# Kernel optimization log

Measured on AMD Instinct MI355X. Metric: run time of the kernel, lower is better.

The kernel has to match this reference:

```python
import jax, jax.numpy as jnp
import numpy as np

KERNEL_MUL = 2.0
KERNEL_NUM = 5


def _mmd(source, target):
    n = source.shape[0]
    total = jnp.concatenate([source, target], axis=0)          # [2N, D]
    n_samples = total.shape[0]
    # GEMM-based pairwise squared L2 distances (same math as broadcast subtract/square/sum)
    sq = jnp.sum(total * total, axis=-1)                        # [2N]
    L2 = sq[:, None] + sq[None, :] - 2.0 * (total @ total.T)    # [2N, 2N]
    # bandwidth from detached distances (torch uses .data)
    bw = jax.lax.stop_gradient(jnp.sum(L2)) / (n_samples ** 2 - n_samples)
    bw = bw / (KERNEL_MUL ** (KERNEL_NUM // 2))
    kernels = jnp.zeros_like(L2)
    for i in range(KERNEL_NUM):
        kernels = kernels + jnp.exp(-L2 / (bw * KERNEL_MUL ** i))
    XX = kernels[:n, :n]
    YY = kernels[n:, n:]
    XY = kernels[:n, n:]
    YX = kernels[n:, :n]
    return jnp.mean(XX + YY - XY - YX)


def setup_inputs() -> dict:
    key = jax.random.key(0)
    k1, k2 = jax.random.split(key)
    N, D = 4096, 128
    source = jax.random.normal(k1, (N, D), dtype=jnp.float32)
    target = jax.random.normal(k2, (N, D), dtype=jnp.float32)
    return {"source": source, "target": target}


def reference(source, target):
    return _mmd(source, target)
```

## Files before the change

### kernel.cpp

```cpp
#include <hip/hip_runtime.h>

#define D 128
#define N_TILES 2080

typedef __attribute__((ext_vector_type(8))) short short8;
typedef __attribute__((ext_vector_type(4))) float float4v;

static __device__ __forceinline__ unsigned short f2bf(float f) {
    unsigned int u = __float_as_uint(f);
    unsigned int r = (u + 0x7fffu + ((u >> 16) & 1u)) >> 16;
    return (unsigned short)r;
}

template <bool STORE>
__global__ void k_rowsq_convert(const float* __restrict__ src, const float* __restrict__ tgt,
                                float* __restrict__ rowsq, unsigned int* __restrict__ xbf) {
    int wave = threadIdx.x >> 6, lane = threadIdx.x & 63;
    int r = blockIdx.x * 4 + wave;
    const float* Xr = (r < 4096) ? src + (size_t)r * D : tgt + (size_t)(r - 4096) * D;
    float2 f = ((const float2*)Xr)[lane];
    float s = f.x * f.x + f.y * f.y;
    if (STORE) {
        unsigned int lo = f2bf(f.x), hi = f2bf(f.y);
        xbf[r * 64 + lane] = lo | (hi << 16);
    }
    #pragma unroll
    for (int off = 32; off; off >>= 1) s += __shfl_down(s, off);
    if (lane == 0) rowsq[r] = s;
}

__global__ void p2_colpart(const float* __restrict__ src, const float* __restrict__ tgt,
                           float* __restrict__ colpart) {
    int b = blockIdx.x;
    int col = threadIdx.x & 127, half = threadIdx.x >> 7;
    const float* X = (b < 64) ? src + (size_t)(b * 64) * D : tgt + (size_t)((b - 64) * 64) * D;
    float part = 0.f;
    for (int i = 0; i < 32; ++i) part += X[(size_t)(2 * i + half) * D + col];
    __shared__ float cp[2][128];
    cp[half][col] = part;
    __syncthreads();
    if (threadIdx.x < 128) colpart[b * 128 + threadIdx.x] = cp[0][threadIdx.x] + cp[1][threadIdx.x];
}

__global__ void p3_consts(const float* __restrict__ rowsq, const float* __restrict__ colpart,
                          float* __restrict__ wsf) {
    int tid = threadIdx.x;
    __shared__ float red[8];
    float s = 0.f;
    for (int i = 0; i < 32; ++i) s += rowsq[tid + 256 * i];
    #pragma unroll
    for (int off = 32; off; off >>= 1) s += __shfl_down(s, off);
    if ((tid & 63) == 0) red[tid >> 6] = s;
    __syncthreads();
    float sumsq = red[0] + red[1] + red[2] + red[3];

    float v = 0.f;
    if (tid < 128) {
        float sd = 0.f;
        for (int b = 0; b < 128; ++b) sd += colpart[b * 128 + tid];
        v = sd * sd;
    }
    __syncthreads();
    #pragma unroll
    for (int off = 32; off; off >>= 1) v += __shfl_down(v, off);
    if ((tid & 63) == 0) red[4 + (tid >> 6)] = v;
    __syncthreads();
    if (tid == 0) {
        double s2 = (double)red[4] + red[5] + red[6] + red[7];
        double sumL2 = 2.0 * 8192.0 * (double)sumsq - 2.0 * s2;
        double bw = sumL2 / (8192.0 * 8192.0 - 8192.0) / 4.0;
        wsf[4] = (float)(-1.4426950408889634 / (bw * 16.0));
    }
}

template <bool BF16WS>
__global__ __launch_bounds__(256, 2) void mmd_main(const float* __restrict__ src,
                                                   const float* __restrict__ tgt,
                                                   const unsigned short* __restrict__ xbf,
                                                   const float* __restrict__ rowsq,
                                                   const float* __restrict__ wsf,
                                                   float* __restrict__ partial) {
    __shared__ unsigned short ldsA[128 * D];
    __shared__ unsigned short ldsB[128 * D];

    int t = blockIdx.x;
    int bi = (int)((129.0 - sqrt(129.0 * 129.0 - 8.0 * (double)t)) * 0.5);
    auto base = [](int b) { return (b * (129 - b)) >> 1; };
    while (base(bi + 1) <= t) ++bi;
    while (base(bi) > t) --bi;
    int bj = bi + (t - base(bi));

    const int tid = threadIdx.x, lane = tid & 63, wv = tid >> 6;
    const int quad = lane >> 4, mrow = lane & 15;

    if (BF16WS) {
        const unsigned short* XA = xbf + (size_t)bi * 128 * D;
        const unsigned short* XB = xbf + (size_t)bj * 128 * D;
        #pragma unroll
        for (int j = 0; j < 8; ++j) {
            int slot = wv * 512 + j * 64 + lane;
            int rr = slot >> 4, sc = slot & 15;
            int cc = sc ^ (rr & 7);
            const unsigned short* gA = XA + rr * D + cc * 8;
            const unsigned short* gB = XB + rr * D + cc * 8;
            int lbase = (wv * 512 + j * 64) * 8;
            __builtin_amdgcn_global_load_lds((const __attribute__((address_space(1))) void*)gA,
                                             (__attribute__((address_space(3))) void*)&ldsA[lbase],
                                             16, 0, 0);
            __builtin_amdgcn_global_load_lds((const __attribute__((address_space(1))) void*)gB,
                                             (__attribute__((address_space(3))) void*)&ldsB[lbase],
                                             16, 0, 0);
        }
    } else {
        const float* XA = (bi < 32) ? src + (size_t)bi * 128 * D : tgt + (size_t)(bi - 32) * 128 * D;
        const float* XB = (bj < 32) ? src + (size_t)bj * 128 * D : tgt + (size_t)(bj - 32) * 128 * D;
        #pragma unroll
        for (int j = 0; j < 8; ++j) {
            int id = j * 256 + tid;
            int rr = id >> 4, cc = id & 15;
            const float4* pa = (const float4*)(XA + rr * D + cc * 8);
            const float4* pb = (const float4*)(XB + rr * D + cc * 8);
            float4 a0 = pa[0], a1 = pa[1];
            float4 b0 = pb[0], b1 = pb[1];
            int dst = rr * D + (cc ^ (rr & 7)) * 8;
            union { unsigned short u[8]; uint4 v; } ka, kb;
            ka.u[0] = f2bf(a0.x); ka.u[1] = f2bf(a0.y); ka.u[2] = f2bf(a0.z); ka.u[3] = f2bf(a0.w);
            ka.u[4] = f2bf(a1.x); ka.u[5] = f2bf(a1.y); ka.u[6] = f2bf(a1.z); ka.u[7] = f2bf(a1.w);
            kb.u[0] = f2bf(b0.x); kb.u[1] = f2bf(b0.y); kb.u[2] = f2bf(b0.z); kb.u[3] = f2bf(b0.w);
            kb.u[4] = f2bf(b1.x); kb.u[5] = f2bf(b1.y); kb.u[6] = f2bf(b1.z); kb.u[7] = f2bf(b1.w);
            *(uint4*)&ldsA[dst] = ka.v;
            *(uint4*)&ldsB[dst] = kb.v;
        }
    }
    float c4 = wsf[4];
    __syncthreads();

    const int wm = wv & 1, wn = wv >> 1;

    float4v accf[4][4];
    #pragma unroll
    for (int mt = 0; mt < 4; ++mt)
        #pragma unroll
        for (int nt = 0; nt < 4; ++nt)
            accf[mt][nt] = (float4v){0.f, 0.f, 0.f, 0.f};

    const int xkey = (mrow & 7);
    #pragma unroll
    for (int kc = 0; kc < 4; ++kc) {
        const int c = kc * 4 + quad;
        const int co = (c ^ xkey) * 8;
        short8 af[4], bfr[4];
        #pragma unroll
        for (int mt = 0; mt < 4; ++mt)
            af[mt] = *(const short8*)&ldsA[(wm * 64 + mt * 16 + mrow) * D + co];
        #pragma unroll
        for (int nt = 0; nt < 4; ++nt)
            bfr[nt] = *(const short8*)&ldsB[(wn * 64 + nt * 16 + mrow) * D + co];
        #pragma unroll
        for (int mt = 0; mt < 4; ++mt)
            #pragma unroll
            for (int nt = 0; nt < 4; ++nt)
                accf[mt][nt] = __builtin_amdgcn_mfma_f32_16x16x32_bf16(af[mt], bfr[nt], accf[mt][nt], 0, 0, 0);
    }

    const float* rsqA = rowsq + bi * 128;
    const float* rsqB = rowsq + bj * 128;
    float part = 0.f;
    #pragma unroll
    for (int mt = 0; mt < 4; ++mt) {
        float rA[4];
        #pragma unroll
        for (int r = 0; r < 4; ++r) rA[r] = rsqA[wm * 64 + mt * 16 + quad * 4 + r];
        #pragma unroll
        for (int nt = 0; nt < 4; ++nt) {
            float rB = rsqB[wn * 64 + nt * 16 + mrow];
            float4v d = accf[mt][nt];
            #pragma unroll
            for (int r = 0; r < 4; ++r) {
                float L2 = rA[r] + rB - 2.f * d[r];
                float e1 = __builtin_amdgcn_exp2f(L2 * c4);
                float e2 = e1 * e1, e4 = e2 * e2, e8 = e4 * e4, e16 = e8 * e8;
                part += ((e1 + e2) + (e4 + e8)) + e16;
            }
        }
    }
    #pragma unroll
    for (int off = 32; off; off >>= 1) part += __shfl_down(part, off);

    __syncthreads();
    float* red = (float*)ldsA;
    if (lane == 0) red[wv] = part;
    __syncthreads();
    if (tid == 0) {
        float s = (red[0] + red[1]) + (red[2] + red[3]);
        float wgt = ((bi < 32) == (bj < 32)) ? 1.f : -1.f;
        if (bi != bj) wgt *= 2.f;
        partial[blockIdx.x] = wgt * s;
    }
}

__global__ void f_final(const float* __restrict__ partial, float* __restrict__ out) {
    int tid = threadIdx.x, lane = tid & 63;
    double s = 0.0;
    for (int i = tid; i < N_TILES; i += 256) s += (double)partial[i];
    #pragma unroll
    for (int off = 32; off; off >>= 1) s += __shfl_down(s, off);
    __shared__ double r4[4];
    if (lane == 0) r4[tid >> 6] = s;
    __syncthreads();
    if (tid == 0)
        out[0] = (float)(((r4[0] + r4[1]) + (r4[2] + r4[3])) * (1.0 / (4096.0 * 4096.0)));
}

extern "C" void kernel_launch(void* const* d_in, const int* in_sizes, int n_in,
                              void* d_out, int out_size, void* d_ws, size_t ws_size,
                              hipStream_t stream) {
    const float* src = (const float*)d_in[0];
    const float* tgt = (const float*)d_in[1];
    float* wsf = (float*)d_ws;
    float* rowsq = wsf + 16;
    float* colpart = wsf + 8208;
    float* partial = wsf + 24592;
    unsigned int* xbf = (unsigned int*)(wsf + 32768);

    const size_t NEED = 32768u * 4u + 8192u * 128u * 2u;
    if (ws_size >= NEED) {
        hipLaunchKernelGGL((k_rowsq_convert<true>), dim3(2048), dim3(256), 0, stream, src, tgt, rowsq, xbf);
        hipLaunchKernelGGL(p2_colpart, dim3(128), dim3(256), 0, stream, src, tgt, colpart);
        hipLaunchKernelGGL(p3_consts, dim3(1), dim3(256), 0, stream, rowsq, colpart, wsf);
        hipLaunchKernelGGL((mmd_main<true>), dim3(N_TILES), dim3(256), 0, stream,
                           src, tgt, (const unsigned short*)xbf, rowsq, wsf, partial);
        hipLaunchKernelGGL(f_final, dim3(1), dim3(256), 0, stream, partial, (float*)d_out);
    } else {
        hipLaunchKernelGGL((k_rowsq_convert<false>), dim3(2048), dim3(256), 0, stream, src, tgt, rowsq, xbf);
        hipLaunchKernelGGL(p2_colpart, dim3(128), dim3(256), 0, stream, src, tgt, colpart);
        hipLaunchKernelGGL(p3_consts, dim3(1), dim3(256), 0, stream, rowsq, colpart, wsf);
        hipLaunchKernelGGL((mmd_main<false>), dim3(N_TILES), dim3(256), 0, stream,
                           src, tgt, (const unsigned short*)xbf, rowsq, wsf, partial);
        hipLaunchKernelGGL(f_final, dim3(1), dim3(256), 0, stream, partial, (float*)d_out);
    }
}
```

Measured before the change: 94.89 us.

## Fuse preprocessing kernels and fold final reduction into main via last-block atomics

Merges the row-norm/bf16 conversion, column-sum and bandwidth-constant kernels into one stats kernel that accumulates column sums and sum of squares with atomics, with the last block computing the bandwidth constant. The final reduction is folded into the main MMD kernel using a completion counter so the last tile block sums partials. This cuts the launch count from five to a memset plus two kernels, removing launch gaps and tiny serial kernels, but adds atomics, threadfences and a memset. The fallback path for small workspaces is dropped.

```diff
diff --git a/kernel.cpp b/kernel.cpp
--- a/kernel.cpp
+++ b/kernel.cpp
@@ -12,76 +12,72 @@
     return (unsigned short)r;
 }
 
-template <bool STORE>
-__global__ void k_rowsq_convert(const float* __restrict__ src, const float* __restrict__ tgt,
-                                float* __restrict__ rowsq, unsigned int* __restrict__ xbf) {
-    int wave = threadIdx.x >> 6, lane = threadIdx.x & 63;
-    int r = blockIdx.x * 4 + wave;
-    const float* Xr = (r < 4096) ? src + (size_t)r * D : tgt + (size_t)(r - 4096) * D;
-    float2 f = ((const float2*)Xr)[lane];
-    float s = f.x * f.x + f.y * f.y;
-    if (STORE) {
-        unsigned int lo = f2bf(f.x), hi = f2bf(f.y);
-        xbf[r * 64 + lane] = lo | (hi << 16);
-    }
-    #pragma unroll
-    for (int off = 32; off; off >>= 1) s += __shfl_down(s, off);
-    if (lane == 0) rowsq[r] = s;
-}
-
-__global__ void p2_colpart(const float* __restrict__ src, const float* __restrict__ tgt,
-                           float* __restrict__ colpart) {
-    int b = blockIdx.x;
-    int col = threadIdx.x & 127, half = threadIdx.x >> 7;
-    const float* X = (b < 64) ? src + (size_t)(b * 64) * D : tgt + (size_t)((b - 64) * 64) * D;
-    float part = 0.f;
-    for (int i = 0; i < 32; ++i) part += X[(size_t)(2 * i + half) * D + col];
-    __shared__ float cp[2][128];
-    cp[half][col] = part;
-    __syncthreads();
-    if (threadIdx.x < 128) colpart[b * 128 + threadIdx.x] = cp[0][threadIdx.x] + cp[1][threadIdx.x];
-}
-
-__global__ void p3_consts(const float* __restrict__ rowsq, const float* __restrict__ colpart,
-                          float* __restrict__ wsf) {
-    int tid = threadIdx.x;
-    __shared__ float red[8];
-    float s = 0.f;
-    for (int i = 0; i < 32; ++i) s += rowsq[tid + 256 * i];
-    #pragma unroll
-    for (int off = 32; off; off >>= 1) s += __shfl_down(s, off);
-    if ((tid & 63) == 0) red[tid >> 6] = s;
-    __syncthreads();
-    float sumsq = red[0] + red[1] + red[2] + red[3];
-
-    float v = 0.f;
-    if (tid < 128) {
-        float sd = 0.f;
-        for (int b = 0; b < 128; ++b) sd += colpart[b * 128 + tid];
-        v = sd * sd;
-    }
-    __syncthreads();
-    #pragma unroll
-    for (int off = 32; off; off >>= 1) v += __shfl_down(v, off);
-    if ((tid & 63) == 0) red[4 + (tid >> 6)] = v;
-    __syncthreads();
-    if (tid == 0) {
-        double s2 = (double)red[4] + red[5] + red[6] + red[7];
-        double sumL2 = 2.0 * 8192.0 * (double)sumsq - 2.0 * s2;
-        double bw = sumL2 / (8192.0 * 8192.0 - 8192.0) / 4.0;
-        wsf[4] = (float)(-1.4426950408889634 / (bw * 16.0));
-    }
-}
-
-template <bool BF16WS>
-__global__ __launch_bounds__(256, 2) void mmd_main(const float* __restrict__ src,
-                                                   const float* __restrict__ tgt,
-                                                   const unsigned short* __restrict__ xbf,
-                                                   const float* __restrict__ rowsq,
-                                                   const float* __restrict__ wsf,
-                                                   float* __restrict__ partial) {
+
+__global__ __launch_bounds__(256) void k_stats(const float* __restrict__ src,
+                                               const float* __restrict__ tgt,
+                                               float* __restrict__ wsf,
+                                               unsigned int* __restrict__ xbf) {
+    double* sumsq = (double*)wsf;
+    unsigned int* cnt = (unsigned int*)(wsf + 2);
+    float* colsum = wsf + 8;
+    float* rowsq = wsf + 256;
+
+    const int tid = threadIdx.x, lane = tid & 63, wv = tid >> 6;
+    float cx = 0.f, cy = 0.f, sq = 0.f;
+    #pragma unroll
+    for (int i = 0; i < 4; ++i) {
+        int r = blockIdx.x * 16 + wv * 4 + i;
+        const float* Xr = (r < 4096) ? src + (size_t)r * D : tgt + (size_t)(r - 4096) * D;
+        float2 f = ((const float2*)Xr)[lane];
+        xbf[r * 64 + lane] = (unsigned)f2bf(f.x) | ((unsigned)f2bf(f.y) << 16);
+        float s = f.x * f.x + f.y * f.y;
+        sq += s; cx += f.x; cy += f.y;
+        #pragma unroll
+        for (int off = 32; off; off >>= 1) s += __shfl_down(s, off);
+        if (lane == 0) rowsq[r] = s;
+    }
+    __shared__ float csx[4][64], csy[4][64], ssh[4];
+    __shared__ int lastS;
+    float t = sq;
+    #pragma unroll
+    for (int off = 32; off; off >>= 1) t += __shfl_down(t, off);
+    csx[wv][lane] = cx; csy[wv][lane] = cy;
+    if (lane == 0) ssh[wv] = t;
+    __syncthreads();
+    if (wv == 0) {
+        float a = csx[0][lane] + csx[1][lane] + csx[2][lane] + csx[3][lane];
+        float b = csy[0][lane] + csy[1][lane] + csy[2][lane] + csy[3][lane];
+        atomicAdd(&colsum[2 * lane], a);
+        atomicAdd(&colsum[2 * lane + 1], b);
+        if (lane == 0) atomicAdd(sumsq, (double)(ssh[0] + ssh[1] + ssh[2] + ssh[3]));
+        __threadfence();
+        if (lane == 0) lastS = (atomicAdd(cnt, 1u) == 511u) ? 1 : 0;
+    }
+    __syncthreads();
+    if (lastS && wv == 0) {
+        __threadfence();
+        float c0 = colsum[lane], c1 = colsum[64 + lane];
+        float v = c0 * c0 + c1 * c1;
+        #pragma unroll
+        for (int off = 32; off; off >>= 1) v += __shfl_down(v, off);
+        if (lane == 0) {
+            double ss = *sumsq;
+            double sumL2 = 2.0 * 8192.0 * ss - 2.0 * (double)v;
+            double bw = sumL2 / (8192.0 * 8192.0 - 8192.0) / 4.0;
+            wsf[4] = (float)(-1.4426950408889634 / (bw * 16.0));
+        }
+    }
+}
+
+__global__ __launch_bounds__(256, 2) void mmd_main(const unsigned short* __restrict__ xbf,
+                                                   float* __restrict__ wsf,
+                                                   float* __restrict__ out) {
     __shared__ unsigned short ldsA[128 * D];
     __shared__ unsigned short ldsB[128 * D];
+
+    const float* rowsq = wsf + 256;
+    float* partial = wsf + 8448;
+    unsigned int* cnt2 = (unsigned int*)(wsf + 3);
 
     int t = blockIdx.x;
     int bi = (int)((129.0 - sqrt(129.0 * 129.0 - 8.0 * (double)t)) * 0.5);
@@ -93,44 +89,22 @@
     const int tid = threadIdx.x, lane = tid & 63, wv = tid >> 6;
     const int quad = lane >> 4, mrow = lane & 15;
 
-    if (BF16WS) {
-        const unsigned short* XA = xbf + (size_t)bi * 128 * D;
-        const unsigned short* XB = xbf + (size_t)bj * 128 * D;
-        #pragma unroll
-        for (int j = 0; j < 8; ++j) {
-            int slot = wv * 512 + j * 64 + lane;
-            int rr = slot >> 4, sc = slot & 15;
-            int cc = sc ^ (rr & 7);
-            const unsigned short* gA = XA + rr * D + cc * 8;
-            const unsigned short* gB = XB + rr * D + cc * 8;
-            int lbase = (wv * 512 + j * 64) * 8;
-            __builtin_amdgcn_global_load_lds((const __attribute__((address_space(1))) void*)gA,
-                                             (__attribute__((address_space(3))) void*)&ldsA[lbase],
-                                             16, 0, 0);
-            __builtin_amdgcn_global_load_lds((const __attribute__((address_space(1))) void*)gB,
-                                             (__attribute__((address_space(3))) void*)&ldsB[lbase],
-                                             16, 0, 0);
-        }
-    } else {
-        const float* XA = (bi < 32) ? src + (size_t)bi * 128 * D : tgt + (size_t)(bi - 32) * 128 * D;
-        const float* XB = (bj < 32) ? src + (size_t)bj * 128 * D : tgt + (size_t)(bj - 32) * 128 * D;
-        #pragma unroll
-        for (int j = 0; j < 8; ++j) {
-            int id = j * 256 + tid;
-            int rr = id >> 4, cc = id & 15;
-            const float4* pa = (const float4*)(XA + rr * D + cc * 8);
-            const float4* pb = (const float4*)(XB + rr * D + cc * 8);
-            float4 a0 = pa[0], a1 = pa[1];
-            float4 b0 = pb[0], b1 = pb[1];
-            int dst = rr * D + (cc ^ (rr & 7)) * 8;
-            union { unsigned short u[8]; uint4 v; } ka, kb;
-            ka.u[0] = f2bf(a0.x); ka.u[1] = f2bf(a0.y); ka.u[2] = f2bf(a0.z); ka.u[3] = f2bf(a0.w);
-            ka.u[4] = f2bf(a1.x); ka.u[5] = f2bf(a1.y); ka.u[6] = f2bf(a1.z); ka.u[7] = f2bf(a1.w);
-            kb.u[0] = f2bf(b0.x); kb.u[1] = f2bf(b0.y); kb.u[2] = f2bf(b0.z); kb.u[3] = f2bf(b0.w);
-            kb.u[4] = f2bf(b1.x); kb.u[5] = f2bf(b1.y); kb.u[6] = f2bf(b1.z); kb.u[7] = f2bf(b1.w);
-            *(uint4*)&ldsA[dst] = ka.v;
-            *(uint4*)&ldsB[dst] = kb.v;
-        }
+    const unsigned short* XA = xbf + (size_t)bi * 128 * D;
+    const unsigned short* XB = xbf + (size_t)bj * 128 * D;
+    #pragma unroll
+    for (int j = 0; j < 8; ++j) {
+        int slot = wv * 512 + j * 64 + lane;
+        int rr = slot >> 4, sc = slot & 15;
+        int cc = sc ^ (rr & 7);
+        const unsigned short* gA = XA + rr * D + cc * 8;
+        const unsigned short* gB = XB + rr * D + cc * 8;
+        int lbase = (wv * 512 + j * 64) * 8;
+        __builtin_amdgcn_global_load_lds((const __attribute__((address_space(1))) void*)gA,
+                                         (__attribute__((address_space(3))) void*)&ldsA[lbase],
+                                         16, 0, 0);
+        __builtin_amdgcn_global_load_lds((const __attribute__((address_space(1))) void*)gB,
+                                         (__attribute__((address_space(3))) void*)&ldsB[lbase],
+                                         16, 0, 0);
     }
     float c4 = wsf[4];
     __syncthreads();
@@ -189,27 +163,30 @@
 
     __syncthreads();
     float* red = (float*)ldsA;
+    double* dred = (double*)(red + 16);
     if (lane == 0) red[wv] = part;
     __syncthreads();
     if (tid == 0) {
         float s = (red[0] + red[1]) + (red[2] + red[3]);
         float wgt = ((bi < 32) == (bj < 32)) ? 1.f : -1.f;
         if (bi != bj) wgt *= 2.f;
-        partial[blockIdx.x] = wgt * s;
-    }
-}
-
-__global__ void f_final(const float* __restrict__ partial, float* __restrict__ out) {
-    int tid = threadIdx.x, lane = tid & 63;
-    double s = 0.0;
-    for (int i = tid; i < N_TILES; i += 256) s += (double)partial[i];
-    #pragma unroll
-    for (int off = 32; off; off >>= 1) s += __shfl_down(s, off);
-    __shared__ double r4[4];
-    if (lane == 0) r4[tid >> 6] = s;
-    __syncthreads();
-    if (tid == 0)
-        out[0] = (float)(((r4[0] + r4[1]) + (r4[2] + r4[3])) * (1.0 / (4096.0 * 4096.0)));
+        partial[t] = wgt * s;
+        __threadfence();
+        ((int*)red)[8] = (atomicAdd(cnt2, 1u) == (unsigned)(N_TILES - 1)) ? 1 : 0;
+    }
+    __syncthreads();
+    if (((int*)red)[8]) {
+        __threadfence();
+        double s = 0.0;
+        for (int i = tid; i < N_TILES; i += 256) s += (double)partial[i];
+        #pragma unroll
+        for (int off = 32; off; off >>= 1) s += __shfl_down(s, off);
+        if (lane == 0) dred[wv] = s;
+        __syncthreads();
+        if (tid == 0)
+            out[0] = (float)(((dred[0] + dred[1]) + (dred[2] + dred[3])) *
+                             (1.0 / (4096.0 * 4096.0)));
+    }
 }
 
 extern "C" void kernel_launch(void* const* d_in, const int* in_sizes, int n_in,
@@ -218,25 +195,10 @@
     const float* src = (const float*)d_in[0];
     const float* tgt = (const float*)d_in[1];
     float* wsf = (float*)d_ws;
-    float* rowsq = wsf + 16;
-    float* colpart = wsf + 8208;
-    float* partial = wsf + 24592;
-    unsigned int* xbf = (unsigned int*)(wsf + 32768);
-
-    const size_t NEED = 32768u * 4u + 8192u * 128u * 2u;
-    if (ws_size >= NEED) {
-        hipLaunchKernelGGL((k_rowsq_convert<true>), dim3(2048), dim3(256), 0, stream, src, tgt, rowsq, xbf);
-        hipLaunchKernelGGL(p2_colpart, dim3(128), dim3(256), 0, stream, src, tgt, colpart);
-        hipLaunchKernelGGL(p3_consts, dim3(1), dim3(256), 0, stream, rowsq, colpart, wsf);
-        hipLaunchKernelGGL((mmd_main<true>), dim3(N_TILES), dim3(256), 0, stream,
-                           src, tgt, (const unsigned short*)xbf, rowsq, wsf, partial);
-        hipLaunchKernelGGL(f_final, dim3(1), dim3(256), 0, stream, partial, (float*)d_out);
-    } else {
-        hipLaunchKernelGGL((k_rowsq_convert<false>), dim3(2048), dim3(256), 0, stream, src, tgt, rowsq, xbf);
-        hipLaunchKernelGGL(p2_colpart, dim3(128), dim3(256), 0, stream, src, tgt, colpart);
-        hipLaunchKernelGGL(p3_consts, dim3(1), dim3(256), 0, stream, rowsq, colpart, wsf);
-        hipLaunchKernelGGL((mmd_main<false>), dim3(N_TILES), dim3(256), 0, stream,
-                           src, tgt, (const unsigned short*)xbf, rowsq, wsf, partial);
-        hipLaunchKernelGGL(f_final, dim3(1), dim3(256), 0, stream, partial, (float*)d_out);
-    }
-}
+    unsigned int* xbf = (unsigned int*)(wsf + 16384);
+
+    hipMemsetAsync(d_ws, 0, 4096, stream);
+    hipLaunchKernelGGL(k_stats, dim3(512), dim3(256), 0, stream, src, tgt, wsf, xbf);
+    hipLaunchKernelGGL(mmd_main, dim3(N_TILES), dim3(256), 0, stream,
+                       (const unsigned short*)xbf, wsf, (float*)d_out);
+}
```

Result: slower. 157.0 us (+65.5%).
